# Performance work log

Hardware: AMD Instinct MI355X
Metric: run time of the kernel (lower is better)

Reference implementation:

```python
import jax, jax.numpy as jnp
import numpy as np

B, N, E, F, U = 256, 240, 4338, 28, 100
NEG_SLOPE = 0.2  # PyG GATConv default negative_slope


def setup_inputs() -> dict:
    key = jax.random.key(0)
    ks = jax.random.split(key, 13)
    s = 0.05  # xavier-ish scale
    return {
        "inputs": jax.random.normal(ks[0], (B, N * F), jnp.float32),
        "state": jax.random.normal(ks[1], (B, N * U), jnp.float32),
        "edge_src": jax.random.randint(ks[2], (E,), 0, N, jnp.int32),
        "edge_dst": jax.random.randint(ks[3], (E,), 0, N, jnp.int32),
        # GATConv(U+F -> U): linear weight, attention vectors, output bias
        "Wg": jax.random.normal(ks[4], (U, U + F), jnp.float32) * s,
        "att_src": jax.random.normal(ks[5], (U,), jnp.float32) * s,
        "att_dst": jax.random.normal(ks[6], (U,), jnp.float32) * s,
        "gat_bias": jnp.zeros((U,), jnp.float32),
        # bias_1 added in _gc3 (self.biases[(100,)])
        "bias1": jnp.zeros((U,), jnp.float32),
        # GRU1: GRULinear(100, 200); GRU2: GRULinear(100, 100)
        "W_ru": jax.random.normal(ks[7], (U + F, 2 * U), jnp.float32) * s,
        "b_ru": jnp.zeros((2 * U,), jnp.float32),
        "W_c": jax.random.normal(ks[8], (U + F, U), jnp.float32) * s,
        "b_c": jnp.zeros((U,), jnp.float32),
    }


def _gat_gru(inputs, state, src, dst, Wg, att_src, att_dst, gat_bias, bias1,
             W_ru, b_ru, W_c, b_c):
    xi = inputs.reshape(B, N, F)
    xs = state.reshape(B, N, U)
    # _gc3: concat [state, inputs] -> GATConv per sample (vectorized here)
    x = jnp.concatenate([xs, xi], axis=2)                 # [B, N, U+F]
    h = jnp.einsum("bnf,cf->bnc", x, Wg)                  # [B, N, U]
    a_src = h @ att_src                                    # [B, N]
    a_dst = h @ att_dst                                    # [B, N]
    e = jax.nn.leaky_relu(a_src[:, src] + a_dst[:, dst], NEG_SLOPE)  # [B, E+N]
    eT = e.T                                               # [E+N, B]
    emax = jax.ops.segment_max(eT, dst, num_segments=N)    # [N, B]
    ex = jnp.exp(eT - emax[dst])
    denom = jax.ops.segment_sum(ex, dst, num_segments=N)   # [N, B]
    alpha = ex / denom[dst]                                # [E+N, B]
    msgs = h[:, src].transpose(1, 0, 2) * alpha[:, :, None]  # [E+N, B, U]
    agg = jax.ops.segment_sum(msgs, dst, num_segments=N)   # [N, B, U]
    gstate = agg.transpose(1, 0, 2) + gat_bias + bias1     # [B, N, U]
    st = gstate.reshape(B, N * U)
    # GRU gates (GRULinear concatenates [inputs, hidden] on feature dim)
    cat1 = jnp.concatenate([xi, gstate], axis=2).reshape(-1, U + F)
    ru = jax.nn.sigmoid((cat1 @ W_ru + b_ru).reshape(B, N, 2 * U))
    r = ru[..., :U].reshape(B, N * U)
    u = ru[..., U:].reshape(B, N * U)
    cat2 = jnp.concatenate([xi, (r * st).reshape(B, N, U)], axis=2).reshape(-1, U + F)
    c = jnp.tanh(cat2 @ W_c + b_c).reshape(B, N * U)
    return u * st + (1.0 - u) * c


def reference(inputs, state, edge_src, edge_dst, Wg, att_src, att_dst,
              gat_bias, bias1, W_ru, b_ru, W_c, b_c):
    # PyG GATConv default add_self_loops=True
    loops = jnp.arange(N, dtype=edge_src.dtype)
    src = jnp.concatenate([edge_src, loops])
    dst = jnp.concatenate([edge_dst, loops])
    return _gat_gru(inputs, state, src, dst, Wg, att_src, att_dst, gat_bias,
                    bias1, W_ru, b_ru, W_c, b_c)
```

## Files before the change

kernel.cpp:

```cpp
#include <hip/hip_runtime.h>

#define Bb 256
#define Nn 240
#define Ee 4338
#define Ff 28
#define Uu 100
#define Kk 128
#define Mrows (Bb * Nn)
#define ET (Ee + Nn)
#define AS 136

typedef __attribute__((ext_vector_type(8))) short bf16x8;
typedef __attribute__((ext_vector_type(4))) float f32x4;
typedef unsigned short u16;

__device__ __forceinline__ float bf2f(u16 u) {
  union { unsigned int i; float f; } v; v.i = ((unsigned int)u) << 16; return v.f;
}
__device__ __forceinline__ u16 f2bf(float f) {
  union { float ff; unsigned int i; } v; v.ff = f;
  unsigned int x = v.i;
  return (u16)((x + 0x7fffu + ((x >> 16) & 1u)) >> 16);
}
__device__ __forceinline__ void split4(const float4 v, ushort4& h, ushort4& l) {
  u16 h0 = f2bf(v.x), h1 = f2bf(v.y), h2 = f2bf(v.z), h3 = f2bf(v.w);
  h.x = h0; h.y = h1; h.z = h2; h.w = h3;
  l.x = f2bf(v.x - bf2f(h0)); l.y = f2bf(v.y - bf2f(h1));
  l.z = f2bf(v.z - bf2f(h2)); l.w = f2bf(v.w - bf2f(h3));
}

__global__ __launch_bounds__(256) void k_prep(
    const float* __restrict__ Wg, const float* __restrict__ Wru, const float* __restrict__ Wc,
    u16* __restrict__ wgh, u16* __restrict__ wgl,
    u16* __restrict__ wruh, u16* __restrict__ wrul,
    u16* __restrict__ wch, u16* __restrict__ wcl) {
  int gt = blockIdx.x * 256 + threadIdx.x, GS = gridDim.x * 256;
  for (int i = gt; i < 128 * Kk; i += GS) {
    int c = i >> 7, k = i & 127;
    float v = (c < Uu) ? Wg[c * Kk + k] : 0.f;
    u16 h = f2bf(v); wgh[i] = h; wgl[i] = f2bf(v - bf2f(h));
  }
  for (int i = gt; i < 256 * Kk; i += GS) {
    int n = i >> 7, kp = i & 127;
    int k = (kp < Uu) ? (kp + Ff) : (kp - Uu);
    float v = (n < 2 * Uu) ? Wru[k * (2 * Uu) + n] : 0.f;
    u16 h = f2bf(v); wruh[i] = h; wrul[i] = f2bf(v - bf2f(h));
  }
  for (int i = gt; i < 128 * Kk; i += GS) {
    int n = i >> 7, kp = i & 127;
    int k = (kp < Uu) ? (kp + Ff) : (kp - Uu);
    float v = (n < Uu) ? Wc[k * Uu + n] : 0.f;
    u16 h = f2bf(v); wch[i] = h; wcl[i] = f2bf(v - bf2f(h));
  }
}

__global__ __launch_bounds__(256) void k_csr(
    const int* __restrict__ esrc, const int* __restrict__ edst,
    int* __restrict__ coff, int* __restrict__ cslot) {
  __shared__ int cnt[256];
  __shared__ int scan[256];
  __shared__ int cur[Nn];
  int tid = threadIdx.x;
  cnt[tid] = 0;
  __syncthreads();
  for (int e = tid; e < Ee; e += 256) atomicAdd(&cnt[edst[e]], 1);
  __syncthreads();
  int x = (tid < Nn) ? (cnt[tid] + 1) : 0;
  int incl = x;
  scan[tid] = incl;
  __syncthreads();
#pragma unroll
  for (int d = 1; d < 256; d <<= 1) {
    int t = (tid >= d) ? scan[tid - d] : 0;
    __syncthreads();
    incl += t;
    scan[tid] = incl;
    __syncthreads();
  }
  int excl = incl - x;
  if (tid < Nn) { coff[tid] = excl; cur[tid] = excl; }
  if (tid == 0) coff[Nn] = scan[Nn - 1];
  __syncthreads();
  for (int e = tid; e < Ee; e += 256) {
    int d = edst[e];
    cslot[atomicAdd(&cur[d], 1)] = esrc[e];
  }
  for (int n = tid; n < Nn; n += 256) cslot[atomicAdd(&cur[n], 1)] = n;
}

__global__ __launch_bounds__(512, 2) void k_fused(
    const float* __restrict__ stt, const float* __restrict__ inp,
    const u16* __restrict__ wgh, const u16* __restrict__ wgl,
    const float* __restrict__ att_s, const float* __restrict__ att_d,
    const int* __restrict__ coff, const int* __restrict__ cslot,
    const float* __restrict__ gbias, const float* __restrict__ b1,
    const u16* __restrict__ wruh, const u16* __restrict__ wrul,
    const float* __restrict__ bru,
    const u16* __restrict__ wch, const u16* __restrict__ wcl,
    const float* __restrict__ bc,
    float* __restrict__ out) {
  __shared__ float hbuf[Nn * Uu];
  __shared__ u16 ahL[32 * AS];
  __shared__ u16 alL[32 * AS];
  __shared__ float gch[32 * Uu];
  __shared__ u16 ugQ[32 * Uu];
  __shared__ float asrcL[Nn];
  __shared__ float adstL[Nn];
  __shared__ int coffL[Nn + 1];
  __shared__ int cslotL[ET];

  int tid = threadIdx.x;
  int b = blockIdx.x;
  const size_t sbase = (size_t)b * Nn * Uu;
  const size_t ibase = (size_t)b * Nn * Ff;

  for (int i = tid; i < Nn + 1; i += 512) coffL[i] = coff[i];
  for (int i = tid; i < ET; i += 512) cslotL[i] = cslot[i];
  for (int i = tid; i < Nn; i += 512) { asrcL[i] = 0.f; adstL[i] = 0.f; }

  int w = tid >> 6, l = tid & 63, l15 = l & 15, q = l >> 4;
  int cw = w * 16 + l15;
  int llb = l & 31, half = l >> 5;

  float4 gbv = {0.f, 0.f, 0.f, 0.f};
  if (l < 25) {
    int u0 = l * 4;
    gbv.x = gbias[u0 + 0] + b1[u0 + 0];
    gbv.y = gbias[u0 + 1] + b1[u0 + 1];
    gbv.z = gbias[u0 + 2] + b1[u0 + 2];
    gbv.w = gbias[u0 + 3] + b1[u0 + 3];
  }

  f32x4 zero = {0.f, 0.f, 0.f, 0.f};

  {
    bf16x8 wh[4], wl[4];
#pragma unroll
    for (int s = 0; s < 4; ++s) {
      const int o = cw * Kk + s * 32 + q * 8;
      wh[s] = *(const bf16x8*)(wgh + o);
      wl[s] = *(const bf16x8*)(wgl + o);
    }
    float av = (cw < Uu) ? att_s[cw] : 0.f;
    float dv = (cw < Uu) ? att_d[cw] : 0.f;

    for (int ch0 = 0; ch0 < Nn; ch0 += 32) {
      int rows = Nn - ch0; if (rows > 32) rows = 32;
      int nrt = rows >> 4;
      for (int j = tid; j < rows * 32; j += 512) {
        int r = j >> 5, g = j & 31;
        float4 v = (g < 25)
            ? *(const float4*)(stt + sbase + (size_t)(ch0 + r) * Uu + g * 4)
            : *(const float4*)(inp + ibase + (size_t)(ch0 + r) * Ff + (g - 25) * 4);
        ushort4 hh, lo;
        split4(v, hh, lo);
        *(ushort4*)(ahL + r * AS + g * 4) = hh;
        *(ushort4*)(alL + r * AS + g * 4) = lo;
      }
      __syncthreads();
      f32x4 acc[2]; acc[0] = zero; acc[1] = zero;
#pragma unroll
      for (int rt = 0; rt < 2; ++rt) if (rt < nrt) {
#pragma unroll
        for (int s = 0; s < 4; ++s) {
          bf16x8 a = *(const bf16x8*)(ahL + (rt * 16 + l15) * AS + s * 32 + q * 8);
          bf16x8 bb = *(const bf16x8*)(alL + (rt * 16 + l15) * AS + s * 32 + q * 8);
          acc[rt] = __builtin_amdgcn_mfma_f32_16x16x32_bf16(a, wh[s], acc[rt], 0, 0, 0);
          acc[rt] = __builtin_amdgcn_mfma_f32_16x16x32_bf16(bb, wh[s], acc[rt], 0, 0, 0);
          acc[rt] = __builtin_amdgcn_mfma_f32_16x16x32_bf16(a, wl[s], acc[rt], 0, 0, 0);
        }
      }
#pragma unroll
      for (int rt = 0; rt < 2; ++rt) if (rt < nrt) {
#pragma unroll
        for (int i = 0; i < 4; ++i) {
          float v = acc[rt][i];
          int row = rt * 16 + q * 4 + i;
          if (cw < Uu) hbuf[(ch0 + row) * Uu + cw] = v;
          float va = v * av, vd = v * dv;
#pragma unroll
          for (int msk = 1; msk < 16; msk <<= 1) {
            va += __shfl_xor(va, msk, 64);
            vd += __shfl_xor(vd, msk, 64);
          }
          if (l15 == 0) {
            atomicAdd(&asrcL[ch0 + row], va);
            atomicAdd(&adstL[ch0 + row], vd);
          }
        }
      }
      __syncthreads();
    }
  }

  bf16x8 r0h[4], r0l[4], r1h[4], r1l[4], cch[4], ccl[4];
  int cw1 = 128 + cw;
#pragma unroll
  for (int s = 0; s < 4; ++s) {
    const int o0 = cw * Kk + s * 32 + q * 8;
    const int o1 = cw1 * Kk + s * 32 + q * 8;
    r0h[s] = *(const bf16x8*)(wruh + o0);
    r0l[s] = *(const bf16x8*)(wrul + o0);
    r1h[s] = *(const bf16x8*)(wruh + o1);
    r1l[s] = *(const bf16x8*)(wrul + o1);
    cch[s] = *(const bf16x8*)(wch + o0);
    ccl[s] = *(const bf16x8*)(wcl + o0);
  }
  float bru0 = bru[cw];
  float bru1 = (cw1 < 2 * Uu) ? bru[cw1] : 0.f;
  float bcv = (cw < Uu) ? bc[cw] : 0.f;

  for (int ch0 = 0; ch0 < Nn; ch0 += 32) {
    int rows = Nn - ch0; if (rows > 32) rows = 32;
    int nrt = rows >> 4;

    for (int n = ch0 + w; n < ch0 + rows; n += 8) {
      int o0 = coffL[n], deg = coffL[n + 1] - o0;
      float ad = adstL[n];
      float ax = 0.f, ay = 0.f, az = 0.f, aw2 = 0.f, den = 0.f;
      for (int c0 = 0; c0 < deg; c0 += 64) {
        int e = c0 + l;
        float we = 0.f; int s = 0;
        if (e < deg) {
          s = cslotL[o0 + e];
          float sc = asrcL[s] + ad;
          sc = (sc > 0.f) ? sc : 0.2f * sc;
          we = __expf(sc);
        }
        float d = we;
#pragma unroll
        for (int msk = 1; msk < 64; msk <<= 1) d += __shfl_xor(d, msk, 64);
        den += d;
        int cn = deg - c0; if (cn > 64) cn = 64;
        for (int e2 = 0; e2 < cn; e2 += 2) {
          int eh = e2 + half;
          float w2 = __shfl(we, eh, 64);
          int s2 = __shfl(s, eh, 64);
          if ((llb < 25) && eh < cn) {
            const float4 hv = *(const float4*)(hbuf + s2 * Uu + llb * 4);
            ax += w2 * hv.x; ay += w2 * hv.y; az += w2 * hv.z; aw2 += w2 * hv.w;
          }
        }
      }
      ax += __shfl_xor(ax, 32, 64);
      ay += __shfl_xor(ay, 32, 64);
      az += __shfl_xor(az, 32, 64);
      aw2 += __shfl_xor(aw2, 32, 64);
      if (l < 25) {
        float inv = 1.f / den;
        float4 o;
        o.x = ax * inv + gbv.x;
        o.y = ay * inv + gbv.y;
        o.z = az * inv + gbv.z;
        o.w = aw2 * inv + gbv.w;
        *(float4*)(gch + (n - ch0) * Uu + l * 4) = o;
      }
    }
    __syncthreads();

    for (int j = tid; j < rows * 32; j += 512) {
      int r = j >> 5, g = j & 31;
      float4 v = (g < 25)
          ? *(const float4*)(gch + r * Uu + g * 4)
          : *(const float4*)(inp + ibase + (size_t)(ch0 + r) * Ff + (g - 25) * 4);
      ushort4 hh, lo;
      split4(v, hh, lo);
      *(ushort4*)(ahL + r * AS + g * 4) = hh;
      *(ushort4*)(alL + r * AS + g * 4) = lo;
    }
    float sv[2][4];
#pragma unroll
    for (int rt = 0; rt < 2; ++rt) if (rt < nrt) {
#pragma unroll
      for (int i = 0; i < 4; ++i) {
        int row = rt * 16 + q * 4 + i;
        sv[rt][i] = (cw < Uu) ? gch[row * Uu + cw] : 0.f;
      }
    }
    __syncthreads();

    float pr[2][4];
    {
      f32x4 acc[2]; acc[0] = zero; acc[1] = zero;
#pragma unroll
      for (int rt = 0; rt < 2; ++rt) if (rt < nrt) {
#pragma unroll
        for (int s = 0; s < 4; ++s) {
          bf16x8 a = *(const bf16x8*)(ahL + (rt * 16 + l15) * AS + s * 32 + q * 8);
          bf16x8 bb = *(const bf16x8*)(alL + (rt * 16 + l15) * AS + s * 32 + q * 8);
          acc[rt] = __builtin_amdgcn_mfma_f32_16x16x32_bf16(a, r0h[s], acc[rt], 0, 0, 0);
          acc[rt] = __builtin_amdgcn_mfma_f32_16x16x32_bf16(bb, r0h[s], acc[rt], 0, 0, 0);
          acc[rt] = __builtin_amdgcn_mfma_f32_16x16x32_bf16(a, r0l[s], acc[rt], 0, 0, 0);
        }
      }
#pragma unroll
      for (int rt = 0; rt < 2; ++rt) if (rt < nrt) {
#pragma unroll
        for (int i = 0; i < 4; ++i) {
          int row = rt * 16 + q * 4 + i;
          float y = acc[rt][i] + bru0;
          float g = 1.f / (1.f + __expf(-y));
          if (cw < Uu) pr[rt][i] = g * sv[rt][i];
          else ugQ[row * Uu + (cw - Uu)] = (u16)(g * 65535.f + 0.5f);
        }
      }
    }
    {
      f32x4 acc[2]; acc[0] = zero; acc[1] = zero;
#pragma unroll
      for (int rt = 0; rt < 2; ++rt) if (rt < nrt) {
#pragma unroll
        for (int s = 0; s < 4; ++s) {
          bf16x8 a = *(const bf16x8*)(ahL + (rt * 16 + l15) * AS + s * 32 + q * 8);
          bf16x8 bb = *(const bf16x8*)(alL + (rt * 16 + l15) * AS + s * 32 + q * 8);
          acc[rt] = __builtin_amdgcn_mfma_f32_16x16x32_bf16(a, r1h[s], acc[rt], 0, 0, 0);
          acc[rt] = __builtin_amdgcn_mfma_f32_16x16x32_bf16(bb, r1h[s], acc[rt], 0, 0, 0);
          acc[rt] = __builtin_amdgcn_mfma_f32_16x16x32_bf16(a, r1l[s], acc[rt], 0, 0, 0);
        }
      }
#pragma unroll
      for (int rt = 0; rt < 2; ++rt) if (rt < nrt) {
#pragma unroll
        for (int i = 0; i < 4; ++i) {
          int row = rt * 16 + q * 4 + i;
          float y = acc[rt][i] + bru1;
          float g = 1.f / (1.f + __expf(-y));
          if (cw1 < 2 * Uu) ugQ[row * Uu + (cw1 - Uu)] = (u16)(g * 65535.f + 0.5f);
        }
      }
    }
    __syncthreads();

#pragma unroll
    for (int rt = 0; rt < 2; ++rt) if (rt < nrt) {
#pragma unroll
      for (int i = 0; i < 4; ++i) {
        int row = rt * 16 + q * 4 + i;
        if (cw < Uu) {
          float p = pr[rt][i];
          u16 hh = f2bf(p);
          ahL[row * AS + cw] = hh;
          alL[row * AS + cw] = f2bf(p - bf2f(hh));
        }
      }
    }
    __syncthreads();

    {
      f32x4 acc[2]; acc[0] = zero; acc[1] = zero;
#pragma unroll
      for (int rt = 0; rt < 2; ++rt) if (rt < nrt) {
#pragma unroll
        for (int s = 0; s < 4; ++s) {
          bf16x8 a = *(const bf16x8*)(ahL + (rt * 16 + l15) * AS + s * 32 + q * 8);
          bf16x8 bb = *(const bf16x8*)(alL + (rt * 16 + l15) * AS + s * 32 + q * 8);
          acc[rt] = __builtin_amdgcn_mfma_f32_16x16x32_bf16(a, cch[s], acc[rt], 0, 0, 0);
          acc[rt] = __builtin_amdgcn_mfma_f32_16x16x32_bf16(bb, cch[s], acc[rt], 0, 0, 0);
          acc[rt] = __builtin_amdgcn_mfma_f32_16x16x32_bf16(a, ccl[s], acc[rt], 0, 0, 0);
        }
      }
#pragma unroll
      for (int rt = 0; rt < 2; ++rt) if (rt < nrt) {
#pragma unroll
        for (int i = 0; i < 4; ++i) {
          int row = rt * 16 + q * 4 + i;
          if (cw < Uu) {
            float y = acc[rt][i] + bcv;
            float cv = 1.f - 2.f / (__expf(2.f * y) + 1.f);
            float u = (float)ugQ[row * Uu + cw] * (1.f / 65535.f);
            out[sbase + (size_t)(ch0 + row) * Uu + cw] = u * sv[rt][i] + (1.f - u) * cv;
          }
        }
      }
    }
  }
}

extern "C" void kernel_launch(void* const* d_in, const int* in_sizes, int n_in,
                              void* d_out, int out_size, void* d_ws, size_t ws_size,
                              hipStream_t stream) {
  const float* inp   = (const float*)d_in[0];
  const float* stt   = (const float*)d_in[1];
  const int*   esrc  = (const int*)d_in[2];
  const int*   edst  = (const int*)d_in[3];
  const float* Wg    = (const float*)d_in[4];
  const float* att_s = (const float*)d_in[5];
  const float* att_d = (const float*)d_in[6];
  const float* gbias = (const float*)d_in[7];
  const float* b1    = (const float*)d_in[8];
  const float* Wru   = (const float*)d_in[9];
  const float* bru   = (const float*)d_in[10];
  const float* Wc    = (const float*)d_in[11];
  const float* bc    = (const float*)d_in[12];
  float* out = (float*)d_out;

  char* base = (char*)d_ws;
  size_t o = 0;
  auto alloc = [&](size_t bytes) -> void* {
    void* p = base + o;
    o = (o + bytes + 255) & ~(size_t)255;
    return p;
  };
  u16* wgh  = (u16*)alloc(128 * Kk * sizeof(u16));
  u16* wgl  = (u16*)alloc(128 * Kk * sizeof(u16));
  u16* wruh = (u16*)alloc(256 * Kk * sizeof(u16));
  u16* wrul = (u16*)alloc(256 * Kk * sizeof(u16));
  u16* wch  = (u16*)alloc(128 * Kk * sizeof(u16));
  u16* wcl  = (u16*)alloc(128 * Kk * sizeof(u16));
  int* coff  = (int*)alloc((Nn + 1) * sizeof(int));
  int* cslot = (int*)alloc(ET * sizeof(int));

  k_prep<<<32, 256, 0, stream>>>(Wg, Wru, Wc, wgh, wgl, wruh, wrul, wch, wcl);
  k_csr<<<1, 256, 0, stream>>>(esrc, edst, coff, cslot);
  k_fused<<<Bb, 512, 0, stream>>>(stt, inp, wgh, wgl, att_s, att_d, coff, cslot,
                                  gbias, b1, wruh, wrul, bru, wch, wcl, bc, out);
}
```

Before: 230.9 us.

## Double block size so each wave owns one 16-row tile instead of two

Raises the fused kernel from 512 to 1024 threads per block. Waves are now indexed by column tile and row tile, so each wave computes a single 16-row MFMA tile per chunk instead of looping over two. The edge-aggregation loop also spreads nodes over 16 waves. The aim is more parallelism and latency hiding per sample. In exchange, launch bounds of 1024 threads with min 4 blocks tighten the register budget while each wave still holds its full weight fragments, which risks spills, and the large shared-memory footprint may limit residency to one block per CU.

Result: slower. 256.5 us (+11.1%).

```diff
diff --git a/kernel.cpp b/kernel.cpp
--- a/kernel.cpp
+++ b/kernel.cpp
@@ -88,7 +88,7 @@
   for (int n = tid; n < Nn; n += 256) cslot[atomicAdd(&cur[n], 1)] = n;
 }
 
-__global__ __launch_bounds__(512, 2) void k_fused(
+__global__ __launch_bounds__(1024, 4) void k_fused(
     const float* __restrict__ stt, const float* __restrict__ inp,
     const u16* __restrict__ wgh, const u16* __restrict__ wgl,
     const float* __restrict__ att_s, const float* __restrict__ att_d,
@@ -114,12 +114,13 @@
   const size_t sbase = (size_t)b * Nn * Uu;
   const size_t ibase = (size_t)b * Nn * Ff;
 
-  for (int i = tid; i < Nn + 1; i += 512) coffL[i] = coff[i];
-  for (int i = tid; i < ET; i += 512) cslotL[i] = cslot[i];
-  for (int i = tid; i < Nn; i += 512) { asrcL[i] = 0.f; adstL[i] = 0.f; }
+  for (int i = tid; i < Nn + 1; i += 1024) coffL[i] = coff[i];
+  for (int i = tid; i < ET; i += 1024) cslotL[i] = cslot[i];
+  for (int i = tid; i < Nn; i += 1024) { asrcL[i] = 0.f; adstL[i] = 0.f; }
 
   int w = tid >> 6, l = tid & 63, l15 = l & 15, q = l >> 4;
-  int cw = w * 16 + l15;
+  int tile = w & 7, rt0 = w >> 3;
+  int cw = tile * 16 + l15;
   int llb = l & 31, half = l >> 5;
 
   float4 gbv = {0.f, 0.f, 0.f, 0.f};
@@ -146,8 +147,8 @@
 
     for (int ch0 = 0; ch0 < Nn; ch0 += 32) {
       int rows = Nn - ch0; if (rows > 32) rows = 32;
-      int nrt = rows >> 4;
-      for (int j = tid; j < rows * 32; j += 512) {
+      bool actrt = (rt0 * 16 < rows);
+      for (int j = tid; j < rows * 32; j += 1024) {
         int r = j >> 5, g = j & 31;
         float4 v = (g < 25)
             ? *(const float4*)(stt + sbase + (size_t)(ch0 + r) * Uu + g * 4)
@@ -158,24 +159,20 @@
         *(ushort4*)(alL + r * AS + g * 4) = lo;
       }
       __syncthreads();
-      f32x4 acc[2]; acc[0] = zero; acc[1] = zero;
-#pragma unroll
-      for (int rt = 0; rt < 2; ++rt) if (rt < nrt) {
+      f32x4 acc = zero;
+      if (actrt) {
 #pragma unroll
         for (int s = 0; s < 4; ++s) {
-          bf16x8 a = *(const bf16x8*)(ahL + (rt * 16 + l15) * AS + s * 32 + q * 8);
-          bf16x8 bb = *(const bf16x8*)(alL + (rt * 16 + l15) * AS + s * 32 + q * 8);
-          acc[rt] = __builtin_amdgcn_mfma_f32_16x16x32_bf16(a, wh[s], acc[rt], 0, 0, 0);
-          acc[rt] = __builtin_amdgcn_mfma_f32_16x16x32_bf16(bb, wh[s], acc[rt], 0, 0, 0);
-          acc[rt] = __builtin_amdgcn_mfma_f32_16x16x32_bf16(a, wl[s], acc[rt], 0, 0, 0);
-        }
-      }
-#pragma unroll
-      for (int rt = 0; rt < 2; ++rt) if (rt < nrt) {
+          bf16x8 a = *(const bf16x8*)(ahL + (rt0 * 16 + l15) * AS + s * 32 + q * 8);
+          bf16x8 bb = *(const bf16x8*)(alL + (rt0 * 16 + l15) * AS + s * 32 + q * 8);
+          acc = __builtin_amdgcn_mfma_f32_16x16x32_bf16(a, wh[s], acc, 0, 0, 0);
+          acc = __builtin_amdgcn_mfma_f32_16x16x32_bf16(bb, wh[s], acc, 0, 0, 0);
+          acc = __builtin_amdgcn_mfma_f32_16x16x32_bf16(a, wl[s], acc, 0, 0, 0);
+        }
 #pragma unroll
         for (int i = 0; i < 4; ++i) {
-          float v = acc[rt][i];
-          int row = rt * 16 + q * 4 + i;
+          float v = acc[i];
+          int row = rt0 * 16 + q * 4 + i;
           if (cw < Uu) hbuf[(ch0 + row) * Uu + cw] = v;
           float va = v * av, vd = v * dv;
 #pragma unroll
@@ -212,9 +209,9 @@
 
   for (int ch0 = 0; ch0 < Nn; ch0 += 32) {
     int rows = Nn - ch0; if (rows > 32) rows = 32;
-    int nrt = rows >> 4;
-
-    for (int n = ch0 + w; n < ch0 + rows; n += 8) {
+    bool actrt = (rt0 * 16 < rows);
+
+    for (int n = ch0 + w; n < ch0 + rows; n += 16) {
       int o0 = coffL[n], deg = coffL[n + 1] - o0;
       float ad = adstL[n];
       float ax = 0.f, ay = 0.f, az = 0.f, aw2 = 0.f, den = 0.f;
@@ -258,7 +255,7 @@
     }
     __syncthreads();
 
-    for (int j = tid; j < rows * 32; j += 512) {
+    for (int j = tid; j < rows * 32; j += 1024) {
       int r = j >> 5, g = j & 31;
       float4 v = (g < 25)
           ? *(const float4*)(gch + r * Uu + g * 4)
@@ -268,76 +265,60 @@
       *(ushort4*)(ahL + r * AS + g * 4) = hh;
       *(ushort4*)(alL + r * AS + g * 4) = lo;
     }
-    float sv[2][4];
-#pragma unroll
-    for (int rt = 0; rt < 2; ++rt) if (rt < nrt) {
-#pragma unroll
-      for (int i = 0; i < 4; ++i) {
-        int row = rt * 16 + q * 4 + i;
-        sv[rt][i] = (cw < Uu) ? gch[row * Uu + cw] : 0.f;
-      }
-    }
-    __syncthreads();
-
-    float pr[2][4];
-    {
-      f32x4 acc[2]; acc[0] = zero; acc[1] = zero;
-#pragma unroll
-      for (int rt = 0; rt < 2; ++rt) if (rt < nrt) {
-#pragma unroll
-        for (int s = 0; s < 4; ++s) {
-          bf16x8 a = *(const bf16x8*)(ahL + (rt * 16 + l15) * AS + s * 32 + q * 8);
-          bf16x8 bb = *(const bf16x8*)(alL + (rt * 16 + l15) * AS + s * 32 + q * 8);
-          acc[rt] = __builtin_amdgcn_mfma_f32_16x16x32_bf16(a, r0h[s], acc[rt], 0, 0, 0);
-          acc[rt] = __builtin_amdgcn_mfma_f32_16x16x32_bf16(bb, r0h[s], acc[rt], 0, 0, 0);
-          acc[rt] = __builtin_amdgcn_mfma_f32_16x16x32_bf16(a, r0l[s], acc[rt], 0, 0, 0);
-        }
-      }
-#pragma unroll
-      for (int rt = 0; rt < 2; ++rt) if (rt < nrt) {
-#pragma unroll
-        for (int i = 0; i < 4; ++i) {
-          int row = rt * 16 + q * 4 + i;
-          float y = acc[rt][i] + bru0;
-          float g = 1.f / (1.f + __expf(-y));
-          if (cw < Uu) pr[rt][i] = g * sv[rt][i];
-          else ugQ[row * Uu + (cw - Uu)] = (u16)(g * 65535.f + 0.5f);
-        }
-      }
-    }
-    {
-      f32x4 acc[2]; acc[0] = zero; acc[1] = zero;
-#pragma unroll
-      for (int rt = 0; rt < 2; ++rt) if (rt < nrt) {
-#pragma unroll
-        for (int s = 0; s < 4; ++s) {
-          bf16x8 a = *(const bf16x8*)(ahL + (rt * 16 + l15) * AS + s * 32 + q * 8);
-          bf16x8 bb = *(const bf16x8*)(alL + (rt * 16 + l15) * AS + s * 32 + q * 8);
-          acc[rt] = __builtin_amdgcn_mfma_f32_16x16x32_bf16(a, r1h[s], acc[rt], 0, 0, 0);
-          acc[rt] = __builtin_amdgcn_mfma_f32_16x16x32_bf16(bb, r1h[s], acc[rt], 0, 0, 0);
-          acc[rt] = __builtin_amdgcn_mfma_f32_16x16x32_bf16(a, r1l[s], acc[rt], 0, 0, 0);
-        }
-      }
-#pragma unroll
-      for (int rt = 0; rt < 2; ++rt) if (rt < nrt) {
-#pragma unroll
-        for (int i = 0; i < 4; ++i) {
-          int row = rt * 16 + q * 4 + i;
-          float y = acc[rt][i] + bru1;
-          float g = 1.f / (1.f + __expf(-y));
-          if (cw1 < 2 * Uu) ugQ[row * Uu + (cw1 - Uu)] = (u16)(g * 65535.f + 0.5f);
-        }
-      }
-    }
-    __syncthreads();
-
-#pragma unroll
-    for (int rt = 0; rt < 2; ++rt) if (rt < nrt) {
-#pragma unroll
-      for (int i = 0; i < 4; ++i) {
-        int row = rt * 16 + q * 4 + i;
+    float sv[4];
+    if (actrt) {
+#pragma unroll
+      for (int i = 0; i < 4; ++i) {
+        int row = rt0 * 16 + q * 4 + i;
+        sv[i] = (cw < Uu) ? gch[row * Uu + cw] : 0.f;
+      }
+    }
+    __syncthreads();
+
+    float pr[4];
+    if (actrt) {
+      f32x4 acc = zero;
+#pragma unroll
+      for (int s = 0; s < 4; ++s) {
+        bf16x8 a = *(const bf16x8*)(ahL + (rt0 * 16 + l15) * AS + s * 32 + q * 8);
+        bf16x8 bb = *(const bf16x8*)(alL + (rt0 * 16 + l15) * AS + s * 32 + q * 8);
+        acc = __builtin_amdgcn_mfma_f32_16x16x32_bf16(a, r0h[s], acc, 0, 0, 0);
+        acc = __builtin_amdgcn_mfma_f32_16x16x32_bf16(bb, r0h[s], acc, 0, 0, 0);
+        acc = __builtin_amdgcn_mfma_f32_16x16x32_bf16(a, r0l[s], acc, 0, 0, 0);
+      }
+#pragma unroll
+      for (int i = 0; i < 4; ++i) {
+        int row = rt0 * 16 + q * 4 + i;
+        float y = acc[i] + bru0;
+        float g = 1.f / (1.f + __expf(-y));
+        if (cw < Uu) pr[i] = g * sv[i];
+        else ugQ[row * Uu + (cw - Uu)] = (u16)(g * 65535.f + 0.5f);
+      }
+      f32x4 acc1 = zero;
+#pragma unroll
+      for (int s = 0; s < 4; ++s) {
+        bf16x8 a = *(const bf16x8*)(ahL + (rt0 * 16 + l15) * AS + s * 32 + q * 8);
+        bf16x8 bb = *(const bf16x8*)(alL + (rt0 * 16 + l15) * AS + s * 32 + q * 8);
+        acc1 = __builtin_amdgcn_mfma_f32_16x16x32_bf16(a, r1h[s], acc1, 0, 0, 0);
+        acc1 = __builtin_amdgcn_mfma_f32_16x16x32_bf16(bb, r1h[s], acc1, 0, 0, 0);
+        acc1 = __builtin_amdgcn_mfma_f32_16x16x32_bf16(a, r1l[s], acc1, 0, 0, 0);
+      }
+#pragma unroll
+      for (int i = 0; i < 4; ++i) {
+        int row = rt0 * 16 + q * 4 + i;
+        float y = acc1[i] + bru1;
+        float g = 1.f / (1.f + __expf(-y));
+        if (cw1 < 2 * Uu) ugQ[row * Uu + (cw1 - Uu)] = (u16)(g * 65535.f + 0.5f);
+      }
+    }
+    __syncthreads();
+
+    if (actrt) {
+#pragma unroll
+      for (int i = 0; i < 4; ++i) {
+        int row = rt0 * 16 + q * 4 + i;
         if (cw < Uu) {
-          float p = pr[rt][i];
+          float p = pr[i];
           u16 hh = f2bf(p);
           ahL[row * AS + cw] = hh;
           alL[row * AS + cw] = f2bf(p - bf2f(hh));
@@ -346,30 +327,24 @@
     }
     __syncthreads();
 
-    {
-      f32x4 acc[2]; acc[0] = zero; acc[1] = zero;
-#pragma unroll
-      for (int rt = 0; rt < 2; ++rt) if (rt < nrt) {
-#pragma unroll
-        for (int s = 0; s < 4; ++s) {
-          bf16x8 a = *(const bf16x8*)(ahL + (rt * 16 + l15) * AS + s * 32 + q * 8);
-          bf16x8 bb = *(const bf16x8*)(alL + (rt * 16 + l15) * AS + s * 32 + q * 8);
-          acc[rt] = __builtin_amdgcn_mfma_f32_16x16x32_bf16(a, cch[s], acc[rt], 0, 0, 0);
-          acc[rt] = __builtin_amdgcn_mfma_f32_16x16x32_bf16(bb, cch[s], acc[rt], 0, 0, 0);
-          acc[rt] = __builtin_amdgcn_mfma_f32_16x16x32_bf16(a, ccl[s], acc[rt], 0, 0, 0);
-        }
-      }
-#pragma unroll
-      for (int rt = 0; rt < 2; ++rt) if (rt < nrt) {
-#pragma unroll
-        for (int i = 0; i < 4; ++i) {
-          int row = rt * 16 + q * 4 + i;
-          if (cw < Uu) {
-            float y = acc[rt][i] + bcv;
-            float cv = 1.f - 2.f / (__expf(2.f * y) + 1.f);
-            float u = (float)ugQ[row * Uu + cw] * (1.f / 65535.f);
-            out[sbase + (size_t)(ch0 + row) * Uu + cw] = u * sv[rt][i] + (1.f - u) * cv;
-          }
+    if (actrt) {
+      f32x4 acc = zero;
+#pragma unroll
+      for (int s = 0; s < 4; ++s) {
+        bf16x8 a = *(const bf16x8*)(ahL + (rt0 * 16 + l15) * AS + s * 32 + q * 8);
+        bf16x8 bb = *(const bf16x8*)(alL + (rt0 * 16 + l15) * AS + s * 32 + q * 8);
+        acc = __builtin_amdgcn_mfma_f32_16x16x32_bf16(a, cch[s], acc, 0, 0, 0);
+        acc = __builtin_amdgcn_mfma_f32_16x16x32_bf16(bb, cch[s], acc, 0, 0, 0);
+        acc = __builtin_amdgcn_mfma_f32_16x16x32_bf16(a, ccl[s], acc, 0, 0, 0);
+      }
+#pragma unroll
+      for (int i = 0; i < 4; ++i) {
+        int row = rt0 * 16 + q * 4 + i;
+        if (cw < Uu) {
+          float y = acc[i] + bcv;
+          float cv = 1.f - 2.f / (__expf(2.f * y) + 1.f);
+          float u = (float)ugQ[row * Uu + cw] * (1.f / 65535.f);
+          out[sbase + (size_t)(ch0 + row) * Uu + cw] = u * sv[i] + (1.f - u) * cv;
         }
       }
     }
@@ -412,6 +387,6 @@
 
   k_prep<<<32, 256, 0, stream>>>(Wg, Wru, Wc, wgh, wgl, wruh, wrul, wch, wcl);
   k_csr<<<1, 256, 0, stream>>>(esrc, edst, coff, cslot);
-  k_fused<<<Bb, 512, 0, stream>>>(stt, inp, wgh, wgl, att_s, att_d, coff, cslot,
-                                  gbias, b1, wruh, wrul, bru, wch, wcl, bc, out);
-}
+  k_fused<<<Bb, 1024, 0, stream>>>(stt, inp, wgh, wgl, att_s, att_d, coff, cslot,
+                                   gbias, b1, wruh, wrul, bru, wch, wcl, bc, out);
+}
```

## Fold weight bf16 splitting and CSR construction into the fused kernel

Applied to the files above, without the earlier changes.

Removes the separate weight-prep and CSR-build kernels. Each block now builds the CSR adjacency itself in shared memory, using atomics and a scan over the edge lists, and converts the fp32 weights into bf16 hi/lo pairs in registers straight from global memory. This drops two kernel launches and their serial dependency. In exchange, the CSR build is done redundantly in every block, and the GRU weight loads become strided scalar reads instead of vectorized ones. The edge order within each segment now comes from per-block atomics, so the order of floating-point summation may differ.

Measured after the change: 220.1 us. 4.7% less time.

```diff
diff --git a/kernel.cpp b/kernel.cpp
--- a/kernel.cpp
+++ b/kernel.cpp
@@ -6,7 +6,6 @@
 #define Ff 28
 #define Uu 100
 #define Kk 128
-#define Mrows (Bb * Nn)
 #define ET (Ee + Nn)
 #define AS 136
 
@@ -28,76 +27,21 @@
   l.x = f2bf(v.x - bf2f(h0)); l.y = f2bf(v.y - bf2f(h1));
   l.z = f2bf(v.z - bf2f(h2)); l.w = f2bf(v.w - bf2f(h3));
 }
-
-__global__ __launch_bounds__(256) void k_prep(
-    const float* __restrict__ Wg, const float* __restrict__ Wru, const float* __restrict__ Wc,
-    u16* __restrict__ wgh, u16* __restrict__ wgl,
-    u16* __restrict__ wruh, u16* __restrict__ wrul,
-    u16* __restrict__ wch, u16* __restrict__ wcl) {
-  int gt = blockIdx.x * 256 + threadIdx.x, GS = gridDim.x * 256;
-  for (int i = gt; i < 128 * Kk; i += GS) {
-    int c = i >> 7, k = i & 127;
-    float v = (c < Uu) ? Wg[c * Kk + k] : 0.f;
-    u16 h = f2bf(v); wgh[i] = h; wgl[i] = f2bf(v - bf2f(h));
-  }
-  for (int i = gt; i < 256 * Kk; i += GS) {
-    int n = i >> 7, kp = i & 127;
-    int k = (kp < Uu) ? (kp + Ff) : (kp - Uu);
-    float v = (n < 2 * Uu) ? Wru[k * (2 * Uu) + n] : 0.f;
-    u16 h = f2bf(v); wruh[i] = h; wrul[i] = f2bf(v - bf2f(h));
-  }
-  for (int i = gt; i < 128 * Kk; i += GS) {
-    int n = i >> 7, kp = i & 127;
-    int k = (kp < Uu) ? (kp + Ff) : (kp - Uu);
-    float v = (n < Uu) ? Wc[k * Uu + n] : 0.f;
-    u16 h = f2bf(v); wch[i] = h; wcl[i] = f2bf(v - bf2f(h));
-  }
-}
-
-__global__ __launch_bounds__(256) void k_csr(
-    const int* __restrict__ esrc, const int* __restrict__ edst,
-    int* __restrict__ coff, int* __restrict__ cslot) {
-  __shared__ int cnt[256];
-  __shared__ int scan[256];
-  __shared__ int cur[Nn];
-  int tid = threadIdx.x;
-  cnt[tid] = 0;
-  __syncthreads();
-  for (int e = tid; e < Ee; e += 256) atomicAdd(&cnt[edst[e]], 1);
-  __syncthreads();
-  int x = (tid < Nn) ? (cnt[tid] + 1) : 0;
-  int incl = x;
-  scan[tid] = incl;
-  __syncthreads();
-#pragma unroll
-  for (int d = 1; d < 256; d <<= 1) {
-    int t = (tid >= d) ? scan[tid - d] : 0;
-    __syncthreads();
-    incl += t;
-    scan[tid] = incl;
-    __syncthreads();
-  }
-  int excl = incl - x;
-  if (tid < Nn) { coff[tid] = excl; cur[tid] = excl; }
-  if (tid == 0) coff[Nn] = scan[Nn - 1];
-  __syncthreads();
-  for (int e = tid; e < Ee; e += 256) {
-    int d = edst[e];
-    cslot[atomicAdd(&cur[d], 1)] = esrc[e];
-  }
-  for (int n = tid; n < Nn; n += 256) cslot[atomicAdd(&cur[n], 1)] = n;
+__device__ __forceinline__ bf16x8 pack8(ushort4 a, ushort4 b) {
+  bf16x8 r;
+  r[0] = (short)a.x; r[1] = (short)a.y; r[2] = (short)a.z; r[3] = (short)a.w;
+  r[4] = (short)b.x; r[5] = (short)b.y; r[6] = (short)b.z; r[7] = (short)b.w;
+  return r;
 }
 
 __global__ __launch_bounds__(512, 2) void k_fused(
     const float* __restrict__ stt, const float* __restrict__ inp,
-    const u16* __restrict__ wgh, const u16* __restrict__ wgl,
+    const float* __restrict__ Wg,
     const float* __restrict__ att_s, const float* __restrict__ att_d,
-    const int* __restrict__ coff, const int* __restrict__ cslot,
+    const int* __restrict__ esrc, const int* __restrict__ edst,
     const float* __restrict__ gbias, const float* __restrict__ b1,
-    const u16* __restrict__ wruh, const u16* __restrict__ wrul,
-    const float* __restrict__ bru,
-    const u16* __restrict__ wch, const u16* __restrict__ wcl,
-    const float* __restrict__ bc,
+    const float* __restrict__ Wru, const float* __restrict__ bru,
+    const float* __restrict__ Wc, const float* __restrict__ bc,
     float* __restrict__ out) {
   __shared__ float hbuf[Nn * Uu];
   __shared__ u16 ahL[32 * AS];
@@ -108,15 +52,46 @@
   __shared__ float adstL[Nn];
   __shared__ int coffL[Nn + 1];
   __shared__ int cslotL[ET];
+  __shared__ int curL[Nn];
+  __shared__ int scanA[256];
 
   int tid = threadIdx.x;
   int b = blockIdx.x;
   const size_t sbase = (size_t)b * Nn * Uu;
   const size_t ibase = (size_t)b * Nn * Ff;
 
-  for (int i = tid; i < Nn + 1; i += 512) coffL[i] = coff[i];
-  for (int i = tid; i < ET; i += 512) cslotL[i] = cslot[i];
+  if (tid < 256) scanA[tid] = 0;
   for (int i = tid; i < Nn; i += 512) { asrcL[i] = 0.f; adstL[i] = 0.f; }
+  __syncthreads();
+  for (int e = tid; e < Ee; e += 512) atomicAdd(&scanA[edst[e]], 1);
+  __syncthreads();
+  int xv = 0, incl = 0;
+  if (tid < 256) {
+    xv = (tid < Nn) ? (scanA[tid] + 1) : 0;
+    incl = xv;
+  }
+  __syncthreads();
+  if (tid < 256) scanA[tid] = incl;
+  __syncthreads();
+#pragma unroll
+  for (int d = 1; d < 256; d <<= 1) {
+    int t = 0;
+    if (tid < 256 && tid >= d) t = scanA[tid - d];
+    __syncthreads();
+    if (tid < 256) { incl += t; scanA[tid] = incl; }
+    __syncthreads();
+  }
+  if (tid < 256) {
+    int excl = incl - xv;
+    if (tid < Nn) { coffL[tid] = excl; curL[tid] = excl; }
+    if (tid == 0) coffL[Nn] = scanA[Nn - 1];
+  }
+  __syncthreads();
+  for (int e = tid; e < Ee; e += 512) {
+    int d = edst[e];
+    cslotL[atomicAdd(&curL[d], 1)] = esrc[e];
+  }
+  for (int n = tid; n < Nn; n += 512) cslotL[atomicAdd(&curL[n], 1)] = n;
 
   int w = tid >> 6, l = tid & 63, l15 = l & 15, q = l >> 4;
   int cw = w * 16 + l15;
@@ -137,9 +112,16 @@
     bf16x8 wh[4], wl[4];
 #pragma unroll
     for (int s = 0; s < 4; ++s) {
-      const int o = cw * Kk + s * 32 + q * 8;
-      wh[s] = *(const bf16x8*)(wgh + o);
-      wl[s] = *(const bf16x8*)(wgl + o);
+      float4 v0 = {0.f, 0.f, 0.f, 0.f}, v1 = {0.f, 0.f, 0.f, 0.f};
+      if (cw < Uu) {
+        v0 = *(const float4*)(Wg + cw * Kk + s * 32 + q * 8);
+        v1 = *(const float4*)(Wg + cw * Kk + s * 32 + q * 8 + 4);
+      }
+      ushort4 h0, l0, h1, l1;
+      split4(v0, h0, l0);
+      split4(v1, h1, l1);
+      wh[s] = pack8(h0, h1);
+      wl[s] = pack8(l0, l1);
     }
     float av = (cw < Uu) ? att_s[cw] : 0.f;
     float dv = (cw < Uu) ? att_d[cw] : 0.f;
@@ -197,14 +179,21 @@
   int cw1 = 128 + cw;
 #pragma unroll
   for (int s = 0; s < 4; ++s) {
-    const int o0 = cw * Kk + s * 32 + q * 8;
-    const int o1 = cw1 * Kk + s * 32 + q * 8;
-    r0h[s] = *(const bf16x8*)(wruh + o0);
-    r0l[s] = *(const bf16x8*)(wrul + o0);
-    r1h[s] = *(const bf16x8*)(wruh + o1);
-    r1l[s] = *(const bf16x8*)(wrul + o1);
-    cch[s] = *(const bf16x8*)(wch + o0);
-    ccl[s] = *(const bf16x8*)(wcl + o0);
+    int kb = s * 32 + q * 8;
+#pragma unroll
+    for (int j = 0; j < 8; ++j) {
+      int kp = kb + j;
+      int k = (kp < Uu) ? (kp + Ff) : (kp - Uu);
+      float v0 = Wru[k * (2 * Uu) + cw];
+      u16 h0 = f2bf(v0);
+      r0h[s][j] = (short)h0; r0l[s][j] = (short)f2bf(v0 - bf2f(h0));
+      float v1 = (cw1 < 2 * Uu) ? Wru[k * (2 * Uu) + cw1] : 0.f;
+      u16 h1 = f2bf(v1);
+      r1h[s][j] = (short)h1; r1l[s][j] = (short)f2bf(v1 - bf2f(h1));
+      float v2 = (cw < Uu) ? Wc[k * Uu + cw] : 0.f;
+      u16 h2 = f2bf(v2);
+      cch[s][j] = (short)h2; ccl[s][j] = (short)f2bf(v2 - bf2f(h2));
+    }
   }
   float bru0 = bru[cw];
   float bru1 = (cw1 < 2 * Uu) ? bru[cw1] : 0.f;
@@ -394,24 +383,6 @@
   const float* bc    = (const float*)d_in[12];
   float* out = (float*)d_out;
 
-  char* base = (char*)d_ws;
-  size_t o = 0;
-  auto alloc = [&](size_t bytes) -> void* {
-    void* p = base + o;
-    o = (o + bytes + 255) & ~(size_t)255;
-    return p;
-  };
-  u16* wgh  = (u16*)alloc(128 * Kk * sizeof(u16));
-  u16* wgl  = (u16*)alloc(128 * Kk * sizeof(u16));
-  u16* wruh = (u16*)alloc(256 * Kk * sizeof(u16));
-  u16* wrul = (u16*)alloc(256 * Kk * sizeof(u16));
-  u16* wch  = (u16*)alloc(128 * Kk * sizeof(u16));
-  u16* wcl  = (u16*)alloc(128 * Kk * sizeof(u16));
-  int* coff  = (int*)alloc((Nn + 1) * sizeof(int));
-  int* cslot = (int*)alloc(ET * sizeof(int));
-
-  k_prep<<<32, 256, 0, stream>>>(Wg, Wru, Wc, wgh, wgl, wruh, wrul, wch, wcl);
-  k_csr<<<1, 256, 0, stream>>>(esrc, edst, coff, cslot);
-  k_fused<<<Bb, 512, 0, stream>>>(stt, inp, wgh, wgl, att_s, att_d, coff, cslot,
-                                  gbias, b1, wruh, wrul, bru, wch, wcl, bc, out);
-}
+  k_fused<<<Bb, 512, 0, stream>>>(stt, inp, Wg, att_s, att_d, esrc, edst,
+                                  gbias, b1, Wru, bru, Wc, bc, out);
+}
```
